# Kernel optimization log

Measured on AMD Instinct MI355X. Metric: run time of the kernel, lower is better.

The kernel has to match this reference:

```python
import jax, jax.numpy as jnp
import numpy as np

B, N = 16, 512
CFL = 0.5


def _conv(x, k):
    return jax.lax.conv_general_dilated(x, k, (1, 1), 'VALID', dimension_numbers=('NHWC', 'HWIO', 'NHWC'))


def _pad(x, p):  # p = (top, bottom, left, right) spatial pads
    return jnp.pad(x, ((0, 0), (p[0], p[1]), (p[2], p[3]), (0, 0)))


def _t(k):  # transpose(perm=[1,0,2,3]) on an HWIO kernel
    return jnp.transpose(k, (1, 0, 2, 3))


def _amper(E, Hx, Hy, beta, delta, fb, fd, fy, kf, kb, fu, fdn):
    n = N
    s1 = (_pad(beta * _conv(Hy, _t(fb)) + delta * _conv(Hy, _t(fd)) + _conv(Hy, _t(fy)), (2, 2, 2, 2))
          + _pad(_conv(Hy, _t(kf)), (2, 2, 0, n - 1))
          + _pad(_conv(Hy, _t(kb)), (2, 2, n - 1, 0))
          + _pad(_conv(Hy, _t(fu)), (2, 2, 1, n - 2))
          + _pad(_conv(Hy, _t(fdn)), (2, 2, n - 2, 1)))
    s2 = (_pad(beta * _conv(Hx, fb) + delta * _conv(Hx, fd) + _conv(Hx, fy), (2, 2, 2, 2))
          + _pad(_conv(Hx, kf), (0, n - 1, 2, 2))
          + _pad(_conv(Hx, kb), (n - 1, 0, 2, 2))
          + _pad(_conv(Hx, fu), (1, n - 2, 2, 2))
          + _pad(_conv(Hx, fdn), (n - 2, 1, 2, 2)))
    return E + CFL * (s1 - s2)


def _faraday(E, Hx, Hy, beta, delta, fb, fd, fy, kef, keb):
    n = N
    s3 = (_pad(beta * _conv(E, fb) + delta * _conv(E, fd) + _conv(E, fy), (0, 0, 1, 1))
          + _pad(_conv(E, kef), (1, 1, 0, n - 2))[:, 1:-1, :, :]
          + _pad(_conv(E, keb), (1, 1, n - 2, 0))[:, 1:-1, :, :])
    s4 = (_pad(beta * _conv(E, _t(fb)) + delta * _conv(E, _t(fd)) + _conv(E, _t(fy)), (1, 1, 0, 0))
          + _pad(_conv(E, _t(kef)), (0, n - 2, 1, 1))[:, :, 1:-1, :]
          + _pad(_conv(E, _t(keb)), (n - 2, 0, 1, 1))[:, :, 1:-1, :])
    return Hx - CFL * s3, Hy + CFL * s4


def _forward(E1, Hx1, Hy1, beta, delta, fb, fd, fy, kf, kb, fu, fdn, kef, keb):
    E2 = _amper(E1, Hx1, Hy1, beta, delta, fb, fd, fy, kf, kb, fu, fdn)
    Hx2, Hy2 = _faraday(E2, Hx1, Hy1, beta, delta, fb, fd, fy, kef, keb)
    E3 = _amper(E2, Hx2, Hy2, beta, delta, fb, fd, fy, kf, kb, fu, fdn)
    Hx3, Hy3 = _faraday(E3, Hx2, Hy2, beta, delta, fb, fd, fy, kef, keb)
    E4 = _amper(E3, Hx3, Hy3, beta, delta, fb, fd, fy, kf, kb, fu, fdn)
    Hx4, Hy4 = _faraday(E4, Hx3, Hy3, beta, delta, fb, fd, fy, kef, keb)
    return (E2, Hx2, Hy2, E3, Hx3, Hy3, E4, Hx4, Hy4)


def setup_inputs():
    key = jax.random.key(0)
    ks = jax.random.split(key, 16)
    f32 = jnp.float32
    E_shape, Hx_shape, Hy_shape = (B, N + 1, N + 1, 1), (B, N - 1, N, 1), (B, N, N - 1, 1)
    # interior 2D DRP stencils (3x4): 4-tap staggered derivative x 3-tap transverse weights
    fy = np.zeros((3, 4, 1, 1), np.float32)
    fy[1, 1, 0, 0] = -1.0
    fy[1, 2, 0, 0] = 1.0
    fb = (np.outer([1.0, -2.0, 1.0], [0.0, -1.0, 1.0, 0.0]) / 8.0).astype(np.float32).reshape(3, 4, 1, 1)
    fd = (np.outer([0.0, 1.0, 0.0], [1.0, -3.0, 3.0, -1.0]) / 24.0).astype(np.float32).reshape(3, 4, 1, 1)
    rnd = lambda k, s: 0.05 * jax.random.normal(k, s, dtype=f32)
    return {
        'E1': jax.random.normal(ks[0], E_shape, f32),
        'Hx1': jax.random.normal(ks[1], Hx_shape, f32),
        'Hy1': jax.random.normal(ks[2], Hy_shape, f32),
        'E2': jax.random.normal(ks[3], E_shape, f32),
        'Hx2': jax.random.normal(ks[4], Hx_shape, f32),
        'Hy2': jax.random.normal(ks[5], Hy_shape, f32),
        'E3': jax.random.normal(ks[6], E_shape, f32),
        'Hx3': jax.random.normal(ks[7], Hx_shape, f32),
        'Hy3': jax.random.normal(ks[8], Hy_shape, f32),
        'beta': jnp.zeros((), f32),
        'delta': jnp.asarray([0.37], f32),
        'filter_beta': jnp.asarray(fb),
        'filter_delta': jnp.asarray(fd),
        'filter_yee': jnp.asarray(fy),
        'kernel_forward': rnd(ks[9], (N - 2, 4, 1, 1)),
        'kernel_backward': rnd(ks[10], (N - 2, 4, 1, 1)),
        'fourth_up': rnd(ks[11], (N - 2, 4, 1, 1)),
        'fourth_down': rnd(ks[12], (N - 2, 4, 1, 1)),
        'kernel_e_forward': rnd(ks[13], (3, N, 1, 1)),
        'kernel_e_backward': rnd(ks[14], (3, N, 1, 1)),
    }


def reference(E1, Hx1, Hy1, E2, Hx2, Hy2, E3, Hx3, Hy3, beta, delta, filter_beta, filter_delta, filter_yee, kernel_forward, kernel_backward, fourth_up, fourth_down, kernel_e_forward, kernel_e_backward):
    # Note: the original layer unpacks E2..Hy3 but never uses them.
    return _forward(E1, Hx1, Hy1, beta, delta, filter_beta, filter_delta, filter_yee,
                    kernel_forward, kernel_backward, fourth_up, fourth_down,
                    kernel_e_forward, kernel_e_backward)
```

## Files before the change

### kernel.cpp

```cpp
#include <hip/hip_runtime.h>

#define NB 16
#define NN 512
#define NP 513
#define NM 511
#define CFLc 0.5f

#define SE (NP*NP)
#define SHX (NM*NN)
#define SHY (NN*NM)

#define WS_BIG 0
#define WS_SMALL (16*16*6*512)
#define WS_TOT (WS_SMALL + 16*512*6)

__device__ __forceinline__ float dot4(float4 a, float4 b) {
    return a.x*b.x + a.y*b.y + a.z*b.z + a.w*b.w;
}

__device__ __forceinline__ void ld5(const float* __restrict__ a, int mb, float4* cr) {
    const float4* a4 = (const float4*)a;
    #pragma unroll
    for (int t = 0; t < 5; t++) {
        int idx = mb - 1 + t;
        if (idx >= 0 && idx <= 509) cr[t] = a4[idx];
        else cr[t] = make_float4(0.f, 0.f, 0.f, 0.f);
    }
}

__global__ __launch_bounds__(512, 4) void k_step1(
    const float* __restrict__ E, const float* __restrict__ Hx, const float* __restrict__ Hy,
    const float* __restrict__ beta, const float* __restrict__ delta,
    const float* __restrict__ fb, const float* __restrict__ fd, const float* __restrict__ fy,
    const float* __restrict__ kf, const float* __restrict__ kb,
    const float* __restrict__ fu, const float* __restrict__ fdn,
    float* __restrict__ ws, float* __restrict__ Eout)
{
    __shared__ float s_hy[7][512];
    __shared__ float s_hx[6][512];
    __shared__ float s_strip[8][6];
    __shared__ float gsm[12];

    int bid = blockIdx.x;
    int tid = threadIdx.x;

    if (bid < 256) {
        int b = bid >> 4;
        int chunk = bid & 15;
        int j = tid;
        if (j > 508) return;
        int p0 = chunk * 32;
        int p1 = min(510, p0 + 32);
        const float* Hxb = Hx + (size_t)b*SHX;
        float akf0=0,akf1=0,akb0=0,akb1=0,afu0=0,afu1=0,afd0=0,afd1=0;
        float r0v[4], r1v[4];
        #pragma unroll
        for (int q = 0; q < 4; q++) r0v[q] = Hxb[(size_t)p0*NN + j + q];
        for (int p = p0; p < p1; p++) {
            #pragma unroll
            for (int q = 0; q < 4; q++) r1v[q] = Hxb[(size_t)(p+1)*NN + j + q];
            #pragma unroll
            for (int q = 0; q < 4; q++) {
                float ckf = kf[p*4+q], ckb = kb[p*4+q], cfu = fu[p*4+q], cfd = fdn[p*4+q];
                akf0 += r0v[q]*ckf; akf1 += r1v[q]*ckf;
                akb0 += r0v[q]*ckb; akb1 += r1v[q]*ckb;
                afu0 += r0v[q]*cfu; afu1 += r1v[q]*cfu;
                afd0 += r0v[q]*cfd; afd1 += r1v[q]*cfd;
            }
            #pragma unroll
            for (int q = 0; q < 4; q++) r0v[q] = r1v[q];
        }
        float* o = ws + WS_BIG + (((size_t)b*16 + chunk)*6)*512 + j;
        o[0*512] = akf0;
        o[1*512] = akf1 + afu0;
        o[2*512] = afu1;
        o[3*512] = afd0;
        o[4*512] = afd1 + akb0;
        o[5*512] = akb1;
        return;
    }

    int wrk = bid - 256;
    wrk = (wrk & 7) * 258 + (wrk >> 3);
    int rg = wrk >> 4;
    int b  = wrk & 15;
    int r0 = rg * 4;

    const float* Eb  = E  + (size_t)b*SE;
    const float* Hxb = Hx + (size_t)b*SHX;
    const float* Hyb = Hy + (size_t)b*SHY;
    int c = tid;

    if (tid < 12) gsm[tid] = beta[0]*fb[tid] + delta[0]*fd[tid] + fy[tid];
    #pragma unroll
    for (int k = 0; k < 7; k++) {
        int rm = min(max(r0-2+k, 0), 511);
        s_hy[k][c] = Hyb[(size_t)rm*NM + min(c, 510)];
    }
    #pragma unroll
    for (int k = 0; k < 6; k++) {
        int rm = min(max(r0-2+k, 0), 510);
        s_hx[k][c] = Hxb[(size_t)rm*NN + c];
    }
    __syncthreads();

    {
        int w = tid >> 6, lane = tid & 63;
        int jj = w >> 1;
        int ii = r0 + jj - 2;
        if (ii >= 0 && ii <= 508) {
            int h = w & 1;
            int mb = h*256 + lane*4;
            float4 hv0 = *(const float4*)&s_hy[jj+0][mb];
            float4 hv1 = *(const float4*)&s_hy[jj+1][mb];
            float4 hv2 = *(const float4*)&s_hy[jj+2][mb];
            float4 hv3 = *(const float4*)&s_hy[jj+3][mb];
            float4 hc0 = make_float4(hv0.x, hv1.x, hv2.x, hv3.x);
            float4 hc1 = make_float4(hv0.y, hv1.y, hv2.y, hv3.y);
            float4 hc2 = make_float4(hv0.z, hv1.z, hv2.z, hv3.z);
            float4 hc3 = make_float4(hv0.w, hv1.w, hv2.w, hv3.w);
            float4 cr[5];
            ld5(kf, mb, cr);
            float pkf0 = dot4(hc0,cr[1]) + dot4(hc1,cr[2]) + dot4(hc2,cr[3]) + dot4(hc3,cr[4]);
            float pkf1 = dot4(hc0,cr[0]) + dot4(hc1,cr[1]) + dot4(hc2,cr[2]) + dot4(hc3,cr[3]);
            ld5(fu, mb, cr);
            float pfu0 = dot4(hc0,cr[1]) + dot4(hc1,cr[2]) + dot4(hc2,cr[3]) + dot4(hc3,cr[4]);
            float pfu1 = dot4(hc0,cr[0]) + dot4(hc1,cr[1]) + dot4(hc2,cr[2]) + dot4(hc3,cr[3]);
            ld5(fdn, mb, cr);
            float pfd0 = dot4(hc0,cr[1]) + dot4(hc1,cr[2]) + dot4(hc2,cr[3]) + dot4(hc3,cr[4]);
            float pfd1 = dot4(hc0,cr[0]) + dot4(hc1,cr[1]) + dot4(hc2,cr[2]) + dot4(hc3,cr[3]);
            ld5(kb, mb, cr);
            float pkb0 = dot4(hc0,cr[1]) + dot4(hc1,cr[2]) + dot4(hc2,cr[3]) + dot4(hc3,cr[4]);
            float pkb1 = dot4(hc0,cr[0]) + dot4(hc1,cr[1]) + dot4(hc2,cr[2]) + dot4(hc3,cr[3]);
            float v0 = pkf0;
            float v1 = pkf1 + pfu0;
            float v2 = pfu1;
            float v3 = pfd0;
            float v4 = pfd1 + pkb0;
            float v5 = pkb1;
            #pragma unroll
            for (int off = 32; off > 0; off >>= 1) {
                v0 += __shfl_down(v0, off);
                v1 += __shfl_down(v1, off);
                v2 += __shfl_down(v2, off);
                v3 += __shfl_down(v3, off);
                v4 += __shfl_down(v4, off);
                v5 += __shfl_down(v5, off);
            }
            if (lane == 0) {
                s_strip[w][0]=v0; s_strip[w][1]=v1; s_strip[w][2]=v2;
                s_strip[w][3]=v3; s_strip[w][4]=v4; s_strip[w][5]=v5;
            }
        }
    }
    __syncthreads();

    float g[12];
    #pragma unroll
    for (int i = 0; i < 12; i++) g[i] = gsm[i];

    int cy0 = min(max(c-2,0),510), cy1 = min(max(c-1,0),510), cy2 = min(c,510);
    int cx0 = max(c-2,0), cx1 = max(c-1,0), cx3 = min(c+1,511);
    float hyv[7][3];
    #pragma unroll
    for (int k = 0; k < 7; k++) {
        hyv[k][0]=s_hy[k][cy0]; hyv[k][1]=s_hy[k][cy1]; hyv[k][2]=s_hy[k][cy2];
    }
    float hxv[6][4];
    #pragma unroll
    for (int k = 0; k < 6; k++) {
        hxv[k][0]=s_hx[k][cx0]; hxv[k][1]=s_hx[k][cx1]; hxv[k][2]=s_hx[k][c]; hxv[k][3]=s_hx[k][cx3];
    }

    bool cint = (c >= 2 && c <= 510);
    int cslot = (c==0)?0:(c==1)?1:(c==2)?2:(c==510)?3:(c==511)?4:-1;
    float* Eo = Eout + (size_t)b*SE;

    #pragma unroll
    for (int j2 = 0; j2 < 4; j2++) {
        int r = r0 + j2;
        if (r > 512) break;
        float v = Eb[(size_t)r*NP + c];
        bool rint = (r >= 2 && r <= 510);
        if (rint && cint) {
            float s1 = 0.f, s2 = 0.f;
            #pragma unroll
            for (int p = 0; p < 4; p++)
                s1 += g[p]*hyv[j2+p][0] + g[4+p]*hyv[j2+p][1] + g[8+p]*hyv[j2+p][2];
            #pragma unroll
            for (int p = 0; p < 3; p++)
                s2 += g[p*4+0]*hxv[j2+p][0] + g[p*4+1]*hxv[j2+p][1]
                    + g[p*4+2]*hxv[j2+p][2] + g[p*4+3]*hxv[j2+p][3];
            v += CFLc * (s1 - s2);
        }
        if (rint && cslot >= 0)
            v += CFLc * (s_strip[2*j2][cslot] + s_strip[2*j2+1][cslot]);
        Eo[(size_t)r*NP + c] = v;
        if (c == 511) {
            float v2 = Eb[(size_t)r*NP + 512];
            if (rint) v2 += CFLc * (s_strip[2*j2][5] + s_strip[2*j2+1][5]);
            Eo[(size_t)r*NP + 512] = v2;
        }
    }
}

__global__ __launch_bounds__(512) void k_fix_e(
    const float* __restrict__ ws, float* __restrict__ Eout)
{
    int b = blockIdx.y;
    int which = blockIdx.x;
    int r = (which < 3) ? which : 507 + which;
    int c = 2 + threadIdx.x;
    if (c > 510) return;
    float s = 0.f;
    #pragma unroll
    for (int ch = 0; ch < 16; ch++)
        s += ws[WS_BIG + (((size_t)b*16 + ch)*6 + which)*512 + (c-2)];
    Eout[(size_t)b*SE + (size_t)r*NP + c] -= CFLc * s;
}

__global__ __launch_bounds__(512, 4) void k_step2(
    const float* __restrict__ E, const float* __restrict__ Hx, const float* __restrict__ Hy,
    const float* __restrict__ beta, const float* __restrict__ delta,
    const float* __restrict__ fb, const float* __restrict__ fd, const float* __restrict__ fy,
    const float* __restrict__ kef, const float* __restrict__ keb,
    float* __restrict__ ws, float* __restrict__ Hxout, float* __restrict__ Hyout)
{
    __shared__ float s_e[7][520];
    __shared__ float s_strip2[8][4];
    __shared__ float gsm[12];

    int bid = blockIdx.x;
    int tid = threadIdx.x;

    if (bid < 256) {
        int b = bid >> 4, chunk = bid & 15;
        int c = tid;
        if (c > 510) return;
        int p0 = chunk*32, p1 = p0 + 32;
        const float* Eb = E + (size_t)b*SE;
        float af0=0, af1=0, ab0=0, ab1=0;
        float r0v[3], r1v[3];
        #pragma unroll
        for (int q = 0; q < 3; q++) r0v[q] = Eb[(size_t)p0*NP + c + q];
        for (int p = p0; p < p1; p++) {
            #pragma unroll
            for (int q = 0; q < 3; q++) r1v[q] = Eb[(size_t)(p+1)*NP + c + q];
            float cf0 = kef[p], cf1 = kef[512+p], cf2 = kef[1024+p];
            float cb0 = keb[p], cb1 = keb[512+p], cb2 = keb[1024+p];
            af0 += r0v[0]*cf0 + r0v[1]*cf1 + r0v[2]*cf2;
            af1 += r1v[0]*cf0 + r1v[1]*cf1 + r1v[2]*cf2;
            ab0 += r0v[0]*cb0 + r0v[1]*cb1 + r0v[2]*cb2;
            ab1 += r1v[0]*cb0 + r1v[1]*cb1 + r1v[2]*cb2;
            r0v[0]=r1v[0]; r0v[1]=r1v[1]; r0v[2]=r1v[2];
        }
        float* o = ws + WS_BIG + (((size_t)b*16 + chunk)*4)*512 + c;
        o[0*512] = af0; o[1*512] = af1; o[2*512] = ab0; o[3*512] = ab1;
        return;
    }

    if (tid < 12) gsm[tid] = beta[0]*fb[tid] + delta[0]*fd[tid] + fy[tid];
    int c = tid;

    if (bid < 2304) {
        int wrk = bid - 256;
        wrk = (wrk & 7)*256 + (wrk >> 3);
        int y = wrk >> 4, b = wrk & 15;
        int r0 = y*4;
        const float* Eb = E + (size_t)b*SE;
        #pragma unroll
        for (int k = 0; k < 6; k++) {
            int rm = min(r0+k, 512);
            s_e[k][c] = Eb[(size_t)rm*NP + c];
            if (c == 511) s_e[k][512] = Eb[(size_t)rm*NP + 512];
        }
        __syncthreads();

        {
            int w = tid >> 6, lane = tid & 63;
            int jj = w >> 1, h = w & 1;
            int rr = r0 + jj;
            if (rr <= 510) {
                int mb = h*256 + lane*4;
                int q4 = mb >> 2;
                float4 e0 = *(const float4*)&s_e[jj+0][mb];
                float4 e1 = *(const float4*)&s_e[jj+1][mb];
                float4 e2 = *(const float4*)&s_e[jj+2][mb];
                const float4* kef4 = (const float4*)kef;
                const float4* keb4 = (const float4*)keb;
                float4 f0 = kef4[q4], f1 = kef4[128+q4], f2 = kef4[256+q4];
                float4 b0 = keb4[q4], b1 = keb4[128+q4], b2 = keb4[256+q4];
                float af0 = dot4(e0,f0) + dot4(e1,f1) + dot4(e2,f2);
                float ab0 = dot4(e0,b0) + dot4(e1,b1) + dot4(e2,b2);
                float pw0 = (mb >= 1) ? kef[mb-1]      : 0.f;
                float pw1 = (mb >= 1) ? kef[512+mb-1]  : 0.f;
                float pw2 = (mb >= 1) ? kef[1024+mb-1] : 0.f;
                float af1 = dot4(e0, make_float4(pw0, f0.x, f0.y, f0.z))
                          + dot4(e1, make_float4(pw1, f1.x, f1.y, f1.z))
                          + dot4(e2, make_float4(pw2, f2.x, f2.y, f2.z));
                pw0 = (mb >= 1) ? keb[mb-1]      : 0.f;
                pw1 = (mb >= 1) ? keb[512+mb-1]  : 0.f;
                pw2 = (mb >= 1) ? keb[1024+mb-1] : 0.f;
                float ab1 = dot4(e0, make_float4(pw0, b0.x, b0.y, b0.z))
                          + dot4(e1, make_float4(pw1, b1.x, b1.y, b1.z))
                          + dot4(e2, make_float4(pw2, b2.x, b2.y, b2.z));
                if (mb == 508) {
                    float e512_0 = s_e[jj+0][512];
                    float e512_1 = s_e[jj+1][512];
                    float e512_2 = s_e[jj+2][512];
                    af1 += e512_0*kef[511] + e512_1*kef[1023] + e512_2*kef[1535];
                    ab1 += e512_0*keb[511] + e512_1*keb[1023] + e512_2*keb[1535];
                }
                #pragma unroll
                for (int off = 32; off > 0; off >>= 1) {
                    af0 += __shfl_down(af0, off);
                    af1 += __shfl_down(af1, off);
                    ab0 += __shfl_down(ab0, off);
                    ab1 += __shfl_down(ab1, off);
                }
                if (lane == 0) {
                    s_strip2[w][0]=af0; s_strip2[w][1]=af1;
                    s_strip2[w][2]=ab0; s_strip2[w][3]=ab1;
                }
            }
        }
        __syncthreads();

        float g[12];
        #pragma unroll
        for (int i = 0; i < 12; i++) g[i] = gsm[i];
        int c0 = max(c-1,0), c2i = min(c+1,512), c3i = min(c+2,512);
        float ev[6][4];
        #pragma unroll
        for (int k = 0; k < 6; k++) {
            ev[k][0]=s_e[k][c0]; ev[k][1]=s_e[k][c]; ev[k][2]=s_e[k][c2i]; ev[k][3]=s_e[k][c3i];
        }
        bool cint = (c >= 1 && c <= 510);
        int slot = (c==0)?0:(c==1)?1:(c==510)?2:(c==511)?3:-1;
        const float* Hxb = Hx + (size_t)b*SHX;
        float* Ho = Hxout + (size_t)b*SHX;
        #pragma unroll
        for (int j2 = 0; j2 < 4; j2++) {
            int r = r0 + j2;
            if (r > 510) break;
            float v = Hxb[(size_t)r*NN + c];
            if (cint) {
                float s = 0.f;
                #pragma unroll
                for (int p = 0; p < 3; p++)
                    s += g[p*4+0]*ev[j2+p][0] + g[p*4+1]*ev[j2+p][1]
                       + g[p*4+2]*ev[j2+p][2] + g[p*4+3]*ev[j2+p][3];
                v -= CFLc * s;
            }
            if (slot >= 0)
                v -= CFLc * (s_strip2[2*j2][slot] + s_strip2[2*j2+1][slot]);
            Ho[(size_t)r*NN + c] = v;
        }
    } else {
        int wrk = bid - 2304;
        wrk = (wrk & 7)*256 + (wrk >> 3);
        int y = wrk >> 4, b = wrk & 15;
        int r0 = y*4;
        const float* Eb = E + (size_t)b*SE;
        #pragma unroll
        for (int k = 0; k < 7; k++) {
            int rm = min(max(r0-1+k, 0), 512);
            s_e[k][c] = Eb[(size_t)rm*NP + c];
            if (c == 511) s_e[k][512] = Eb[(size_t)rm*NP + 512];
        }
        __syncthreads();
        if (c > 510) return;

        float g[12];
        #pragma unroll
        for (int i = 0; i < 12; i++) g[i] = gsm[i];
        float ev[7][3];
        #pragma unroll
        for (int k = 0; k < 7; k++) {
            ev[k][0]=s_e[k][c]; ev[k][1]=s_e[k][c+1]; ev[k][2]=s_e[k][c+2];
        }
        const float* Hyb = Hy + (size_t)b*SHY;
        float* Ho = Hyout + (size_t)b*SHY;
        #pragma unroll
        for (int j2 = 0; j2 < 4; j2++) {
            int r = r0 + j2;
            float v = Hyb[(size_t)r*NM + c];
            if (r >= 1 && r <= 510) {
                float s = 0.f;
                #pragma unroll
                for (int p = 0; p < 4; p++)
                    s += g[p]*ev[j2+p][0] + g[4+p]*ev[j2+p][1] + g[8+p]*ev[j2+p][2];
                v += CFLc * s;
            }
            Ho[(size_t)r*NM + c] = v;
        }
    }
}

__global__ __launch_bounds__(512) void k_fix_hy(
    const float* __restrict__ ws, float* __restrict__ Hyout)
{
    int b = blockIdx.y;
    int which = blockIdx.x;
    int r = (which < 2) ? which : 508 + which;
    int c = threadIdx.x;
    if (c > 510) return;
    float s = 0.f;
    #pragma unroll
    for (int ch = 0; ch < 16; ch++)
        s += ws[WS_BIG + (((size_t)b*16 + ch)*4 + which)*512 + c];
    Hyout[(size_t)b*SHY + (size_t)r*NM + c] += CFLc * s;
}


static void run_step(const float* Ein, const float* Hxin, const float* Hyin,
                     float* Eout, float* Hxout, float* Hyout, float* ws,
                     const float* beta, const float* delta,
                     const float* fb, const float* fd, const float* fy,
                     const float* kf, const float* kb, const float* fu, const float* fdn,
                     const float* kef, const float* keb, hipStream_t stream)
{
    dim3 blk(512);
    k_step1<<<dim3(256 + 2064), blk, 0, stream>>>(Ein, Hxin, Hyin, beta, delta,
        fb, fd, fy, kf, kb, fu, fdn, ws, Eout);
    k_fix_e<<<dim3(6, NB), blk, 0, stream>>>(ws, Eout);
    k_step2<<<dim3(256 + 2048 + 2048), blk, 0, stream>>>(Eout, Hxin, Hyin, beta, delta,
        fb, fd, fy, kef, keb, ws, Hxout, Hyout);
    k_fix_hy<<<dim3(4, NB), blk, 0, stream>>>(ws, Hyout);
}

extern "C" void kernel_launch(void* const* d_in, const int* in_sizes, int n_in,
                              void* d_out, int out_size, void* d_ws, size_t ws_size,
                              hipStream_t stream)
{
    const float* E1   = (const float*)d_in[0];
    const float* Hx1  = (const float*)d_in[1];
    const float* Hy1  = (const float*)d_in[2];
    const float* beta = (const float*)d_in[9];
    const float* delta= (const float*)d_in[10];
    const float* fb   = (const float*)d_in[11];
    const float* fd   = (const float*)d_in[12];
    const float* fy   = (const float*)d_in[13];
    const float* kf   = (const float*)d_in[14];
    const float* kb   = (const float*)d_in[15];
    const float* fu   = (const float*)d_in[16];
    const float* fdn  = (const float*)d_in[17];
    const float* kef  = (const float*)d_in[18];
    const float* keb  = (const float*)d_in[19];

    float* out = (float*)d_out;
    float* ws  = (float*)d_ws;
    size_t SEa = (size_t)NB * SE;
    size_t SHa = (size_t)NB * SHX;
    float* E2  = out;
    float* Hx2 = E2  + SEa;
    float* Hy2 = Hx2 + SHa;
    float* E3  = Hy2 + SHa;
    float* Hx3 = E3  + SEa;
    float* Hy3 = Hx3 + SHa;
    float* E4  = Hy3 + SHa;
    float* Hx4 = E4  + SEa;
    float* Hy4 = Hx4 + SHa;

    run_step(E1, Hx1, Hy1, E2, Hx2, Hy2, ws, beta, delta, fb, fd, fy, kf, kb, fu, fdn, kef, keb, stream);
    run_step(E2, Hx2, Hy2, E3, Hx3, Hy3, ws, beta, delta, fb, fd, fy, kf, kb, fu, fdn, kef, keb, stream);
    run_step(E3, Hx3, Hy3, E4, Hx4, Hy4, ws, beta, delta, fb, fd, fy, kf, kb, fu, fdn, kef, keb, stream);
}
```

Measured before the change: 485.7 us.

## Make stencil blocks persistent over four row-groups with register-prefetched double-buffered LDS

```diff
diff --git a/kernel.cpp b/kernel.cpp
--- a/kernel.cpp
+++ b/kernel.cpp
@@ -36,8 +36,8 @@
     const float* __restrict__ fu, const float* __restrict__ fdn,
     float* __restrict__ ws, float* __restrict__ Eout)
 {
-    __shared__ float s_hy[7][512];
-    __shared__ float s_hx[6][512];
+    __shared__ float s_hy[2][7][512];
+    __shared__ float s_hx[2][6][512];
     __shared__ float s_strip[8][6];
     __shared__ float gsm[12];
 
@@ -81,10 +81,11 @@
     }
 
     int wrk = bid - 256;
-    wrk = (wrk & 7) * 258 + (wrk >> 3);
-    int rg = wrk >> 4;
-    int b  = wrk & 15;
-    int r0 = rg * 4;
+    wrk = (wrk & 7) * 66 + (wrk >> 3);
+    int b  = wrk / 33;
+    int jb = wrk - b*33;
+    int rgBase = jb * 4;
+    int T = min(4, 129 - rgBase);
 
     const float* Eb  = E  + (size_t)b*SE;
     const float* Hxb = Hx + (size_t)b*SHX;
@@ -92,115 +93,141 @@
     int c = tid;
 
     if (tid < 12) gsm[tid] = beta[0]*fb[tid] + delta[0]*fd[tid] + fy[tid];
-    #pragma unroll
-    for (int k = 0; k < 7; k++) {
-        int rm = min(max(r0-2+k, 0), 511);
-        s_hy[k][c] = Hyb[(size_t)rm*NM + min(c, 510)];
-    }
-    #pragma unroll
-    for (int k = 0; k < 6; k++) {
-        int rm = min(max(r0-2+k, 0), 510);
-        s_hx[k][c] = Hxb[(size_t)rm*NN + c];
-    }
-    __syncthreads();
-
-    {
-        int w = tid >> 6, lane = tid & 63;
-        int jj = w >> 1;
-        int ii = r0 + jj - 2;
-        if (ii >= 0 && ii <= 508) {
-            int h = w & 1;
-            int mb = h*256 + lane*4;
-            float4 hv0 = *(const float4*)&s_hy[jj+0][mb];
-            float4 hv1 = *(const float4*)&s_hy[jj+1][mb];
-            float4 hv2 = *(const float4*)&s_hy[jj+2][mb];
-            float4 hv3 = *(const float4*)&s_hy[jj+3][mb];
-            float4 hc0 = make_float4(hv0.x, hv1.x, hv2.x, hv3.x);
-            float4 hc1 = make_float4(hv0.y, hv1.y, hv2.y, hv3.y);
-            float4 hc2 = make_float4(hv0.z, hv1.z, hv2.z, hv3.z);
-            float4 hc3 = make_float4(hv0.w, hv1.w, hv2.w, hv3.w);
-            float4 cr[5];
-            ld5(kf, mb, cr);
-            float pkf0 = dot4(hc0,cr[1]) + dot4(hc1,cr[2]) + dot4(hc2,cr[3]) + dot4(hc3,cr[4]);
-            float pkf1 = dot4(hc0,cr[0]) + dot4(hc1,cr[1]) + dot4(hc2,cr[2]) + dot4(hc3,cr[3]);
-            ld5(fu, mb, cr);
-            float pfu0 = dot4(hc0,cr[1]) + dot4(hc1,cr[2]) + dot4(hc2,cr[3]) + dot4(hc3,cr[4]);
-            float pfu1 = dot4(hc0,cr[0]) + dot4(hc1,cr[1]) + dot4(hc2,cr[2]) + dot4(hc3,cr[3]);
-            ld5(fdn, mb, cr);
-            float pfd0 = dot4(hc0,cr[1]) + dot4(hc1,cr[2]) + dot4(hc2,cr[3]) + dot4(hc3,cr[4]);
-            float pfd1 = dot4(hc0,cr[0]) + dot4(hc1,cr[1]) + dot4(hc2,cr[2]) + dot4(hc3,cr[3]);
-            ld5(kb, mb, cr);
-            float pkb0 = dot4(hc0,cr[1]) + dot4(hc1,cr[2]) + dot4(hc2,cr[3]) + dot4(hc3,cr[4]);
-            float pkb1 = dot4(hc0,cr[0]) + dot4(hc1,cr[1]) + dot4(hc2,cr[2]) + dot4(hc3,cr[3]);
-            float v0 = pkf0;
-            float v1 = pkf1 + pfu0;
-            float v2 = pfu1;
-            float v3 = pfd0;
-            float v4 = pfd1 + pkb0;
-            float v5 = pkb1;
-            #pragma unroll
-            for (int off = 32; off > 0; off >>= 1) {
-                v0 += __shfl_down(v0, off);
-                v1 += __shfl_down(v1, off);
-                v2 += __shfl_down(v2, off);
-                v3 += __shfl_down(v3, off);
-                v4 += __shfl_down(v4, off);
-                v5 += __shfl_down(v5, off);
-            }
-            if (lane == 0) {
-                s_strip[w][0]=v0; s_strip[w][1]=v1; s_strip[w][2]=v2;
-                s_strip[w][3]=v3; s_strip[w][4]=v4; s_strip[w][5]=v5;
-            }
-        }
-    }
-    __syncthreads();
-
-    float g[12];
-    #pragma unroll
-    for (int i = 0; i < 12; i++) g[i] = gsm[i];
-
-    int cy0 = min(max(c-2,0),510), cy1 = min(max(c-1,0),510), cy2 = min(c,510);
-    int cx0 = max(c-2,0), cx1 = max(c-1,0), cx3 = min(c+1,511);
-    float hyv[7][3];
-    #pragma unroll
-    for (int k = 0; k < 7; k++) {
-        hyv[k][0]=s_hy[k][cy0]; hyv[k][1]=s_hy[k][cy1]; hyv[k][2]=s_hy[k][cy2];
-    }
-    float hxv[6][4];
-    #pragma unroll
-    for (int k = 0; k < 6; k++) {
-        hxv[k][0]=s_hx[k][cx0]; hxv[k][1]=s_hx[k][cx1]; hxv[k][2]=s_hx[k][c]; hxv[k][3]=s_hx[k][cx3];
-    }
-
-    bool cint = (c >= 2 && c <= 510);
-    int cslot = (c==0)?0:(c==1)?1:(c==2)?2:(c==510)?3:(c==511)?4:-1;
-    float* Eo = Eout + (size_t)b*SE;
-
-    #pragma unroll
-    for (int j2 = 0; j2 < 4; j2++) {
-        int r = r0 + j2;
-        if (r > 512) break;
-        float v = Eb[(size_t)r*NP + c];
-        bool rint = (r >= 2 && r <= 510);
-        if (rint && cint) {
-            float s1 = 0.f, s2 = 0.f;
-            #pragma unroll
-            for (int p = 0; p < 4; p++)
-                s1 += g[p]*hyv[j2+p][0] + g[4+p]*hyv[j2+p][1] + g[8+p]*hyv[j2+p][2];
-            #pragma unroll
-            for (int p = 0; p < 3; p++)
-                s2 += g[p*4+0]*hxv[j2+p][0] + g[p*4+1]*hxv[j2+p][1]
-                    + g[p*4+2]*hxv[j2+p][2] + g[p*4+3]*hxv[j2+p][3];
-            v += CFLc * (s1 - s2);
-        }
-        if (rint && cslot >= 0)
-            v += CFLc * (s_strip[2*j2][cslot] + s_strip[2*j2+1][cslot]);
-        Eo[(size_t)r*NP + c] = v;
-        if (c == 511) {
-            float v2 = Eb[(size_t)r*NP + 512];
-            if (rint) v2 += CFLc * (s_strip[2*j2][5] + s_strip[2*j2+1][5]);
-            Eo[(size_t)r*NP + 512] = v2;
-        }
+
+    float rHy[7], rHx[6], rE[4];
+    auto ldregs = [&](int r0) {
+        #pragma unroll
+        for (int k = 0; k < 7; k++) {
+            int rm = min(max(r0-2+k, 0), 511);
+            rHy[k] = Hyb[(size_t)rm*NM + min(c, 510)];
+        }
+        #pragma unroll
+        for (int k = 0; k < 6; k++) {
+            int rm = min(max(r0-2+k, 0), 510);
+            rHx[k] = Hxb[(size_t)rm*NN + c];
+        }
+        #pragma unroll
+        for (int j = 0; j < 4; j++)
+            rE[j] = Eb[(size_t)min(r0+j, 512)*NP + c];
+    };
+
+    ldregs(rgBase*4);
+
+    for (int t = 0; t < T; ++t) {
+        int buf = t & 1;
+        int r0 = (rgBase + t) * 4;
+
+        #pragma unroll
+        for (int k = 0; k < 7; k++) s_hy[buf][k][c] = rHy[k];
+        #pragma unroll
+        for (int k = 0; k < 6; k++) s_hx[buf][k][c] = rHx[k];
+        float ev[4];
+        #pragma unroll
+        for (int j = 0; j < 4; j++) ev[j] = rE[j];
+        __syncthreads();
+
+        if (t+1 < T) ldregs(r0 + 4);
+
+        {
+            int w = tid >> 6, lane = tid & 63;
+            int jj = w >> 1;
+            int ii = r0 + jj - 2;
+            if (ii >= 0 && ii <= 508) {
+                int h = w & 1;
+                int mb = h*256 + lane*4;
+                float4 hv0 = *(const float4*)&s_hy[buf][jj+0][mb];
+                float4 hv1 = *(const float4*)&s_hy[buf][jj+1][mb];
+                float4 hv2 = *(const float4*)&s_hy[buf][jj+2][mb];
+                float4 hv3 = *(const float4*)&s_hy[buf][jj+3][mb];
+                float4 hc0 = make_float4(hv0.x, hv1.x, hv2.x, hv3.x);
+                float4 hc1 = make_float4(hv0.y, hv1.y, hv2.y, hv3.y);
+                float4 hc2 = make_float4(hv0.z, hv1.z, hv2.z, hv3.z);
+                float4 hc3 = make_float4(hv0.w, hv1.w, hv2.w, hv3.w);
+                float4 cr[5];
+                ld5(kf, mb, cr);
+                float pkf0 = dot4(hc0,cr[1]) + dot4(hc1,cr[2]) + dot4(hc2,cr[3]) + dot4(hc3,cr[4]);
+                float pkf1 = dot4(hc0,cr[0]) + dot4(hc1,cr[1]) + dot4(hc2,cr[2]) + dot4(hc3,cr[3]);
+                ld5(fu, mb, cr);
+                float pfu0 = dot4(hc0,cr[1]) + dot4(hc1,cr[2]) + dot4(hc2,cr[3]) + dot4(hc3,cr[4]);
+                float pfu1 = dot4(hc0,cr[0]) + dot4(hc1,cr[1]) + dot4(hc2,cr[2]) + dot4(hc3,cr[3]);
+                ld5(fdn, mb, cr);
+                float pfd0 = dot4(hc0,cr[1]) + dot4(hc1,cr[2]) + dot4(hc2,cr[3]) + dot4(hc3,cr[4]);
+                float pfd1 = dot4(hc0,cr[0]) + dot4(hc1,cr[1]) + dot4(hc2,cr[2]) + dot4(hc3,cr[3]);
+                ld5(kb, mb, cr);
+                float pkb0 = dot4(hc0,cr[1]) + dot4(hc1,cr[2]) + dot4(hc2,cr[3]) + dot4(hc3,cr[4]);
+                float pkb1 = dot4(hc0,cr[0]) + dot4(hc1,cr[1]) + dot4(hc2,cr[2]) + dot4(hc3,cr[3]);
+                float v0 = pkf0;
+                float v1 = pkf1 + pfu0;
+                float v2 = pfu1;
+                float v3 = pfd0;
+                float v4 = pfd1 + pkb0;
+                float v5 = pkb1;
+                #pragma unroll
+                for (int off = 32; off > 0; off >>= 1) {
+                    v0 += __shfl_down(v0, off);
+                    v1 += __shfl_down(v1, off);
+                    v2 += __shfl_down(v2, off);
+                    v3 += __shfl_down(v3, off);
+                    v4 += __shfl_down(v4, off);
+                    v5 += __shfl_down(v5, off);
+                }
+                if (lane == 0) {
+                    s_strip[w][0]=v0; s_strip[w][1]=v1; s_strip[w][2]=v2;
+                    s_strip[w][3]=v3; s_strip[w][4]=v4; s_strip[w][5]=v5;
+                }
+            }
+        }
+        __syncthreads();
+
+        float g[12];
+        #pragma unroll
+        for (int i = 0; i < 12; i++) g[i] = gsm[i];
+
+        int cy0 = min(max(c-2,0),510), cy1 = min(max(c-1,0),510), cy2 = min(c,510);
+        int cx0 = max(c-2,0), cx1 = max(c-1,0), cx3 = min(c+1,511);
+        float hyv[7][3];
+        #pragma unroll
+        for (int k = 0; k < 7; k++) {
+            hyv[k][0]=s_hy[buf][k][cy0]; hyv[k][1]=s_hy[buf][k][cy1]; hyv[k][2]=s_hy[buf][k][cy2];
+        }
+        float hxv[6][4];
+        #pragma unroll
+        for (int k = 0; k < 6; k++) {
+            hxv[k][0]=s_hx[buf][k][cx0]; hxv[k][1]=s_hx[buf][k][cx1];
+            hxv[k][2]=s_hx[buf][k][c];   hxv[k][3]=s_hx[buf][k][cx3];
+        }
+
+        bool cint = (c >= 2 && c <= 510);
+        int cslot = (c==0)?0:(c==1)?1:(c==2)?2:(c==510)?3:(c==511)?4:-1;
+        float* Eo = Eout + (size_t)b*SE;
+
+        #pragma unroll
+        for (int j2 = 0; j2 < 4; j2++) {
+            int r = r0 + j2;
+            if (r > 512) break;
+            float v = ev[j2];
+            bool rint = (r >= 2 && r <= 510);
+            if (rint && cint) {
+                float s1 = 0.f, s2 = 0.f;
+                #pragma unroll
+                for (int p = 0; p < 4; p++)
+                    s1 += g[p]*hyv[j2+p][0] + g[4+p]*hyv[j2+p][1] + g[8+p]*hyv[j2+p][2];
+                #pragma unroll
+                for (int p = 0; p < 3; p++)
+                    s2 += g[p*4+0]*hxv[j2+p][0] + g[p*4+1]*hxv[j2+p][1]
+                        + g[p*4+2]*hxv[j2+p][2] + g[p*4+3]*hxv[j2+p][3];
+                v += CFLc * (s1 - s2);
+            }
+            if (rint && cslot >= 0)
+                v += CFLc * (s_strip[2*j2][cslot] + s_strip[2*j2+1][cslot]);
+            Eo[(size_t)r*NP + c] = v;
+            if (c == 511) {
+                float v2 = Eb[(size_t)r*NP + 512];
+                if (rint) v2 += CFLc * (s_strip[2*j2][5] + s_strip[2*j2+1][5]);
+                Eo[(size_t)r*NP + 512] = v2;
+            }
+        }
+        __syncthreads();
     }
 }
 
@@ -226,7 +253,7 @@
     const float* __restrict__ kef, const float* __restrict__ keb,
     float* __restrict__ ws, float* __restrict__ Hxout, float* __restrict__ Hyout)
 {
-    __shared__ float s_e[7][520];
+    __shared__ float s_e[2][7][520];
     __shared__ float s_strip2[8][4];
     __shared__ float gsm[12];
 
@@ -262,137 +289,185 @@
     if (tid < 12) gsm[tid] = beta[0]*fb[tid] + delta[0]*fd[tid] + fy[tid];
     int c = tid;
 
-    if (bid < 2304) {
+    if (bid < 768) {
         int wrk = bid - 256;
-        wrk = (wrk & 7)*256 + (wrk >> 3);
-        int y = wrk >> 4, b = wrk & 15;
-        int r0 = y*4;
+        wrk = (wrk & 7)*64 + (wrk >> 3);
+        int b = wrk >> 5;
+        int yBase = (wrk & 31) * 4;
         const float* Eb = E + (size_t)b*SE;
-        #pragma unroll
-        for (int k = 0; k < 6; k++) {
-            int rm = min(r0+k, 512);
-            s_e[k][c] = Eb[(size_t)rm*NP + c];
-            if (c == 511) s_e[k][512] = Eb[(size_t)rm*NP + 512];
-        }
-        __syncthreads();
-
-        {
-            int w = tid >> 6, lane = tid & 63;
-            int jj = w >> 1, h = w & 1;
-            int rr = r0 + jj;
-            if (rr <= 510) {
-                int mb = h*256 + lane*4;
-                int q4 = mb >> 2;
-                float4 e0 = *(const float4*)&s_e[jj+0][mb];
-                float4 e1 = *(const float4*)&s_e[jj+1][mb];
-                float4 e2 = *(const float4*)&s_e[jj+2][mb];
-                const float4* kef4 = (const float4*)kef;
-                const float4* keb4 = (const float4*)keb;
-                float4 f0 = kef4[q4], f1 = kef4[128+q4], f2 = kef4[256+q4];
-                float4 b0 = keb4[q4], b1 = keb4[128+q4], b2 = keb4[256+q4];
-                float af0 = dot4(e0,f0) + dot4(e1,f1) + dot4(e2,f2);
-                float ab0 = dot4(e0,b0) + dot4(e1,b1) + dot4(e2,b2);
-                float pw0 = (mb >= 1) ? kef[mb-1]      : 0.f;
-                float pw1 = (mb >= 1) ? kef[512+mb-1]  : 0.f;
-                float pw2 = (mb >= 1) ? kef[1024+mb-1] : 0.f;
-                float af1 = dot4(e0, make_float4(pw0, f0.x, f0.y, f0.z))
-                          + dot4(e1, make_float4(pw1, f1.x, f1.y, f1.z))
-                          + dot4(e2, make_float4(pw2, f2.x, f2.y, f2.z));
-                pw0 = (mb >= 1) ? keb[mb-1]      : 0.f;
-                pw1 = (mb >= 1) ? keb[512+mb-1]  : 0.f;
-                pw2 = (mb >= 1) ? keb[1024+mb-1] : 0.f;
-                float ab1 = dot4(e0, make_float4(pw0, b0.x, b0.y, b0.z))
-                          + dot4(e1, make_float4(pw1, b1.x, b1.y, b1.z))
-                          + dot4(e2, make_float4(pw2, b2.x, b2.y, b2.z));
-                if (mb == 508) {
-                    float e512_0 = s_e[jj+0][512];
-                    float e512_1 = s_e[jj+1][512];
-                    float e512_2 = s_e[jj+2][512];
-                    af1 += e512_0*kef[511] + e512_1*kef[1023] + e512_2*kef[1535];
-                    ab1 += e512_0*keb[511] + e512_1*keb[1023] + e512_2*keb[1535];
+        const float* Hxb = Hx + (size_t)b*SHX;
+        float* Ho = Hxout + (size_t)b*SHX;
+
+        float rE[6], rX[6], rIn[4];
+        auto ldregs = [&](int r0) {
+            #pragma unroll
+            for (int k = 0; k < 6; k++) {
+                int rm = min(r0+k, 512);
+                rE[k] = Eb[(size_t)rm*NP + c];
+                rX[k] = (c == 511) ? Eb[(size_t)rm*NP + 512] : 0.f;
+            }
+            #pragma unroll
+            for (int j = 0; j < 4; j++)
+                rIn[j] = Hxb[(size_t)min(r0+j, 510)*NN + c];
+        };
+        ldregs(yBase*4);
+
+        for (int t = 0; t < 4; ++t) {
+            int buf = t & 1;
+            int r0 = (yBase + t) * 4;
+            #pragma unroll
+            for (int k = 0; k < 6; k++) {
+                s_e[buf][k][c] = rE[k];
+                if (c == 511) s_e[buf][k][512] = rX[k];
+            }
+            float vin[4];
+            #pragma unroll
+            for (int j = 0; j < 4; j++) vin[j] = rIn[j];
+            __syncthreads();
+            if (t+1 < 4) ldregs(r0 + 4);
+
+            {
+                int w = tid >> 6, lane = tid & 63;
+                int jj = w >> 1, h = w & 1;
+                int rr = r0 + jj;
+                if (rr <= 510) {
+                    int mb = h*256 + lane*4;
+                    int q4 = mb >> 2;
+                    float4 e0 = *(const float4*)&s_e[buf][jj+0][mb];
+                    float4 e1 = *(const float4*)&s_e[buf][jj+1][mb];
+                    float4 e2 = *(const float4*)&s_e[buf][jj+2][mb];
+                    const float4* kef4 = (const float4*)kef;
+                    const float4* keb4 = (const float4*)keb;
+                    float4 f0 = kef4[q4], f1 = kef4[128+q4], f2 = kef4[256+q4];
+                    float4 b0 = keb4[q4], b1 = keb4[128+q4], b2 = keb4[256+q4];
+                    float af0 = dot4(e0,f0) + dot4(e1,f1) + dot4(e2,f2);
+                    float ab0 = dot4(e0,b0) + dot4(e1,b1) + dot4(e2,b2);
+                    float pw0 = (mb >= 1) ? kef[mb-1]      : 0.f;
+                    float pw1 = (mb >= 1) ? kef[512+mb-1]  : 0.f;
+                    float pw2 = (mb >= 1) ? kef[1024+mb-1] : 0.f;
+                    float af1 = dot4(e0, make_float4(pw0, f0.x, f0.y, f0.z))
+                              + dot4(e1, make_float4(pw1, f1.x, f1.y, f1.z))
+                              + dot4(e2, make_float4(pw2, f2.x, f2.y, f2.z));
+                    pw0 = (mb >= 1) ? keb[mb-1]      : 0.f;
+                    pw1 = (mb >= 1) ? keb[512+mb-1]  : 0.f;
+                    pw2 = (mb >= 1) ? keb[1024+mb-1] : 0.f;
+                    float ab1 = dot4(e0, make_float4(pw0, b0.x, b0.y, b0.z))
+                              + dot4(e1, make_float4(pw1, b1.x, b1.y, b1.z))
+                              + dot4(e2, make_float4(pw2, b2.x, b2.y, b2.z));
+                    if (mb == 508) {
+                        float e512_0 = s_e[buf][jj+0][512];
+                        float e512_1 = s_e[buf][jj+1][512];
+                        float e512_2 = s_e[buf][jj+2][512];
+                        af1 += e512_0*kef[511] + e512_1*kef[1023] + e512_2*kef[1535];
+                        ab1 += e512_0*keb[511] + e512_1*keb[1023] + e512_2*keb[1535];
+                    }
+                    #pragma unroll
+                    for (int off = 32; off > 0; off >>= 1) {
+                        af0 += __shfl_down(af0, off);
+                        af1 += __shfl_down(af1, off);
+                        ab0 += __shfl_down(ab0, off);
+                        ab1 += __shfl_down(ab1, off);
+                    }
+                    if (lane == 0) {
+                        s_strip2[w][0]=af0; s_strip2[w][1]=af1;
+                        s_strip2[w][2]=ab0; s_strip2[w][3]=ab1;
+                    }
+                }
+            }
+            __syncthreads();
+
+            float g[12];
+            #pragma unroll
+            for (int i = 0; i < 12; i++) g[i] = gsm[i];
+            int c0 = max(c-1,0), c2i = min(c+1,512), c3i = min(c+2,512);
+            float evv[6][4];
+            #pragma unroll
+            for (int k = 0; k < 6; k++) {
+                evv[k][0]=s_e[buf][k][c0]; evv[k][1]=s_e[buf][k][c];
+                evv[k][2]=s_e[buf][k][c2i]; evv[k][3]=s_e[buf][k][c3i];
+            }
+            bool cint = (c >= 1 && c <= 510);
+            int slot = (c==0)?0:(c==1)?1:(c==510)?2:(c==511)?3:-1;
+            #pragma unroll
+            for (int j2 = 0; j2 < 4; j2++) {
+                int r = r0 + j2;
+                if (r > 510) break;
+                float v = vin[j2];
+                if (cint) {
+                    float s = 0.f;
+                    #pragma unroll
+                    for (int p = 0; p < 3; p++)
+                        s += g[p*4+0]*evv[j2+p][0] + g[p*4+1]*evv[j2+p][1]
+                           + g[p*4+2]*evv[j2+p][2] + g[p*4+3]*evv[j2+p][3];
+                    v -= CFLc * s;
+                }
+                if (slot >= 0)
+                    v -= CFLc * (s_strip2[2*j2][slot] + s_strip2[2*j2+1][slot]);
+                Ho[(size_t)r*NN + c] = v;
+            }
+            __syncthreads();
+        }
+    } else {
+        int wrk = bid - 768;
+        wrk = (wrk & 7)*64 + (wrk >> 3);
+        int b = wrk >> 5;
+        int yBase = (wrk & 31) * 4;
+        const float* Eb = E + (size_t)b*SE;
+        const float* Hyb = Hy + (size_t)b*SHY;
+        float* Ho = Hyout + (size_t)b*SHY;
+
+        float rE[7], rX[7], rIn[4];
+        auto ldregs = [&](int r0) {
+            #pragma unroll
+            for (int k = 0; k < 7; k++) {
+                int rm = min(max(r0-1+k, 0), 512);
+                rE[k] = Eb[(size_t)rm*NP + c];
+                rX[k] = (c == 511) ? Eb[(size_t)rm*NP + 512] : 0.f;
+            }
+            #pragma unroll
+            for (int j = 0; j < 4; j++)
+                rIn[j] = Hyb[(size_t)(r0+j)*NM + min(c, 510)];
+        };
+        ldregs(yBase*4);
+
+        for (int t = 0; t < 4; ++t) {
+            int buf = t & 1;
+            int r0 = (yBase + t) * 4;
+            #pragma unroll
+            for (int k = 0; k < 7; k++) {
+                s_e[buf][k][c] = rE[k];
+                if (c == 511) s_e[buf][k][512] = rX[k];
+            }
+            float vin[4];
+            #pragma unroll
+            for (int j = 0; j < 4; j++) vin[j] = rIn[j];
+            __syncthreads();
+            if (t+1 < 4) ldregs(r0 + 4);
+
+            if (c <= 510) {
+                float g[12];
+                #pragma unroll
+                for (int i = 0; i < 12; i++) g[i] = gsm[i];
+                float evv[7][3];
+                #pragma unroll
+                for (int k = 0; k < 7; k++) {
+                    evv[k][0]=s_e[buf][k][c]; evv[k][1]=s_e[buf][k][c+1]; evv[k][2]=s_e[buf][k][c+2];
                 }
                 #pragma unroll
-                for (int off = 32; off > 0; off >>= 1) {
-                    af0 += __shfl_down(af0, off);
-                    af1 += __shfl_down(af1, off);
-                    ab0 += __shfl_down(ab0, off);
-                    ab1 += __shfl_down(ab1, off);
+                for (int j2 = 0; j2 < 4; j2++) {
+                    int r = r0 + j2;
+                    float v = vin[j2];
+                    if (r >= 1 && r <= 510) {
+                        float s = 0.f;
+                        #pragma unroll
+                        for (int p = 0; p < 4; p++)
+                            s += g[p]*evv[j2+p][0] + g[4+p]*evv[j2+p][1] + g[8+p]*evv[j2+p][2];
+                        v += CFLc * s;
+                    }
+                    Ho[(size_t)r*NM + c] = v;
                 }
-                if (lane == 0) {
-                    s_strip2[w][0]=af0; s_strip2[w][1]=af1;
-                    s_strip2[w][2]=ab0; s_strip2[w][3]=ab1;
-                }
-            }
-        }
-        __syncthreads();
-
-        float g[12];
-        #pragma unroll
-        for (int i = 0; i < 12; i++) g[i] = gsm[i];
-        int c0 = max(c-1,0), c2i = min(c+1,512), c3i = min(c+2,512);
-        float ev[6][4];
-        #pragma unroll
-        for (int k = 0; k < 6; k++) {
-            ev[k][0]=s_e[k][c0]; ev[k][1]=s_e[k][c]; ev[k][2]=s_e[k][c2i]; ev[k][3]=s_e[k][c3i];
-        }
-        bool cint = (c >= 1 && c <= 510);
-        int slot = (c==0)?0:(c==1)?1:(c==510)?2:(c==511)?3:-1;
-        const float* Hxb = Hx + (size_t)b*SHX;
-        float* Ho = Hxout + (size_t)b*SHX;
-        #pragma unroll
-        for (int j2 = 0; j2 < 4; j2++) {
-            int r = r0 + j2;
-            if (r > 510) break;
-            float v = Hxb[(size_t)r*NN + c];
-            if (cint) {
-                float s = 0.f;
-                #pragma unroll
-                for (int p = 0; p < 3; p++)
-                    s += g[p*4+0]*ev[j2+p][0] + g[p*4+1]*ev[j2+p][1]
-                       + g[p*4+2]*ev[j2+p][2] + g[p*4+3]*ev[j2+p][3];
-                v -= CFLc * s;
-            }
-            if (slot >= 0)
-                v -= CFLc * (s_strip2[2*j2][slot] + s_strip2[2*j2+1][slot]);
-            Ho[(size_t)r*NN + c] = v;
-        }
-    } else {
-        int wrk = bid - 2304;
-        wrk = (wrk & 7)*256 + (wrk >> 3);
-        int y = wrk >> 4, b = wrk & 15;
-        int r0 = y*4;
-        const float* Eb = E + (size_t)b*SE;
-        #pragma unroll
-        for (int k = 0; k < 7; k++) {
-            int rm = min(max(r0-1+k, 0), 512);
-            s_e[k][c] = Eb[(size_t)rm*NP + c];
-            if (c == 511) s_e[k][512] = Eb[(size_t)rm*NP + 512];
-        }
-        __syncthreads();
-        if (c > 510) return;
-
-        float g[12];
-        #pragma unroll
-        for (int i = 0; i < 12; i++) g[i] = gsm[i];
-        float ev[7][3];
-        #pragma unroll
-        for (int k = 0; k < 7; k++) {
-            ev[k][0]=s_e[k][c]; ev[k][1]=s_e[k][c+1]; ev[k][2]=s_e[k][c+2];
-        }
-        const float* Hyb = Hy + (size_t)b*SHY;
-        float* Ho = Hyout + (size_t)b*SHY;
-        #pragma unroll
-        for (int j2 = 0; j2 < 4; j2++) {
-            int r = r0 + j2;
-            float v = Hyb[(size_t)r*NM + c];
-            if (r >= 1 && r <= 510) {
-                float s = 0.f;
-                #pragma unroll
-                for (int p = 0; p < 4; p++)
-                    s += g[p]*ev[j2+p][0] + g[4+p]*ev[j2+p][1] + g[8+p]*ev[j2+p][2];
-                v += CFLc * s;
-            }
-            Ho[(size_t)r*NM + c] = v;
+            }
+            __syncthreads();
         }
     }
 }
@@ -421,10 +496,10 @@
                      const float* kef, const float* keb, hipStream_t stream)
 {
     dim3 blk(512);
-    k_step1<<<dim3(256 + 2064), blk, 0, stream>>>(Ein, Hxin, Hyin, beta, delta,
+    k_step1<<<dim3(256 + 528), blk, 0, stream>>>(Ein, Hxin, Hyin, beta, delta,
         fb, fd, fy, kf, kb, fu, fdn, ws, Eout);
     k_fix_e<<<dim3(6, NB), blk, 0, stream>>>(ws, Eout);
-    k_step2<<<dim3(256 + 2048 + 2048), blk, 0, stream>>>(Eout, Hxin, Hyin, beta, delta,
+    k_step2<<<dim3(256 + 512 + 512), blk, 0, stream>>>(Eout, Hxin, Hyin, beta, delta,
         fb, fd, fy, kef, keb, ws, Hxout, Hyout);
     k_fix_hy<<<dim3(4, NB), blk, 0, stream>>>(ws, Hyout);
 }
```

Result: slower. 618.8 us (+27.4%).
